# Optimization experiments

Hardware: AMD Instinct MI355X
Metric: run time of the kernel (lower is better)

## Reference

```python
import jax, jax.numpy as jnp
import numpy as np

EMBED_DIM = 512
KDIM = 64
VDIM = 64


def setup_inputs() -> dict:
    key = jax.random.key(0)
    kx, kq, kk, kv = jax.random.split(key, 4)
    B, S = 4, 4096
    x = jax.random.normal(kx, (B, S, EMBED_DIM), dtype=jnp.float32)
    # nn.Linear(embed_dim, out) weight has shape [out, embed_dim]
    WQ = jax.random.normal(kq, (KDIM, EMBED_DIM), dtype=jnp.float32) * (EMBED_DIM ** -0.5)
    WK = jax.random.normal(kk, (KDIM, EMBED_DIM), dtype=jnp.float32) * (EMBED_DIM ** -0.5)
    WV = jax.random.normal(kv, (VDIM, EMBED_DIM), dtype=jnp.float32) * (EMBED_DIM ** -0.5)
    return {"x": x, "WQ": WQ, "WK": WK, "WV": WV}


def reference(x, WQ, WK, WV):
    # q,k: [B,S,kdim]; v: [B,S,vdim] (self-attention: x[0] is x[-1])
    q = jnp.einsum('bse,ke->bsk', x, WQ)
    k = jnp.einsum('bse,ke->bsk', x, WK)
    v = jnp.einsum('bse,ve->bsv', x, WV)
    scale = k.shape[-1] ** -0.5
    scores = jnp.einsum('bqk,bsk->bqs', q, k) * scale  # [B,S,S]
    # dropout p=0.0 -> identity; masked branch in source is a no-op (non-in-place masked_fill discarded)
    attn = jax.nn.softmax(scores, axis=-1)
    out = jnp.einsum('bqs,bsv->bqv', attn, v)  # [B,S,vdim]
    return out
```

## Files before the change

### kernel.cpp

```cpp
#include <hip/hip_runtime.h>

#define BATCH 4
#define SEQ   4096
#define EMB   512
#define HD    64

typedef __attribute__((ext_vector_type(8))) short short8;
typedef __attribute__((ext_vector_type(4))) float floatx4;

static __device__ __forceinline__ unsigned short f2bf(float f) {
  unsigned u = __builtin_bit_cast(unsigned, f);
  u += 0x7fffu + ((u >> 16) & 1u);
  return (unsigned short)(u >> 16);
}
static __device__ __forceinline__ float bf2f(unsigned short h) {
  unsigned u = ((unsigned)h) << 16;
  return __builtin_bit_cast(float, u);
}
static __device__ __forceinline__ unsigned pack_hi16(float lo, float hi) {
#if __has_builtin(__builtin_amdgcn_perm)
  return __builtin_amdgcn_perm(__builtin_bit_cast(unsigned, hi),
                               __builtin_bit_cast(unsigned, lo), 0x07060302u);
#else
  return (__builtin_bit_cast(unsigned, lo) >> 16) |
         (__builtin_bit_cast(unsigned, hi) & 0xffff0000u);
#endif
}
static __device__ __forceinline__ unsigned pack_f16(float a, float b) {
#if __has_builtin(__builtin_amdgcn_cvt_pkrtz)
  typedef __fp16 fp16v2 __attribute__((ext_vector_type(2)));
  fp16v2 h = __builtin_amdgcn_cvt_pkrtz(a, b);
  return __builtin_bit_cast(unsigned, h);
#else
  _Float16 ha = (_Float16)a, hb = (_Float16)b;
  return (unsigned)__builtin_bit_cast(unsigned short, ha) |
         ((unsigned)__builtin_bit_cast(unsigned short, hb) << 16);
#endif
}
static __device__ __forceinline__ float f16_to_f32(unsigned short bits) {
  _Float16 h = __builtin_bit_cast(_Float16, bits);
  return (float)h;
}

__global__ __launch_bounds__(256) void convw_kernel(
    const float* __restrict__ WQ, const float* __restrict__ WK,
    const float* __restrict__ WV, unsigned short* __restrict__ Wpk)
{
  int t = blockIdx.x * 256 + threadIdx.x;
  int p    = t >> 12;
  int w    = (t >> 10) & 3;
  int kc   = (t >> 6) & 15;
  int lane = t & 63;
  int lr = lane & 15, g = lane >> 4;
  const float* src = (p == 0) ? WQ : ((p == 1) ? WK : WV);
  const float4* s4 = (const float4*)(src + (16 * w + lr) * EMB + kc * 32 + 8 * g);
  float4 a = s4[0], b = s4[1];
  float vv[8] = {a.x, a.y, a.z, a.w, b.x, b.y, b.z, b.w};
  short8 o;
#pragma unroll
  for (int j = 0; j < 8; ++j) {
    unsigned short h = f2bf(vv[j]);
    o[j] = (p == 3) ? (short)f2bf(vv[j] - bf2f(h)) : (short)h;
  }
  *(short8*)(Wpk + (size_t)t * 8) = o;
}

#define XST 40

__global__ __launch_bounds__(256) void proj_kernel(
    const float* __restrict__ x,
    const unsigned short* __restrict__ Wpk,
    unsigned short* __restrict__ Qb,
    unsigned short* __restrict__ Kb,
    unsigned short* __restrict__ VTb)
{
  __shared__ __align__(16) unsigned short Xh[2][32 * XST];
  __shared__ __align__(16) unsigned short Xl[2][32 * XST];

  const int tid  = threadIdx.x;
  const int lane = tid & 63;
  const int w    = tid >> 6;
  const int lr   = lane & 15, g = lane >> 4;
  const long rowBase = (long)blockIdx.x * 32;

  floatx4 accQ[2], accK[2], accV[2];
#pragma unroll
  for (int rt = 0; rt < 2; ++rt) {
    floatx4 z = {0.f, 0.f, 0.f, 0.f};
    accQ[rt] = z; accK[rt] = z; accV[rt] = z;
  }

  const int srow = tid >> 3;
  const int sc   = 4 * (tid & 7);
  const float* xbase = x + (rowBase + srow) * EMB + sc;

  auto stage_write = [&](float4 v, int buf) {
    float vv[4] = {v.x, v.y, v.z, v.w};
    ushort4 hi, lo;
#pragma unroll
    for (int i = 0; i < 4; ++i) {
      unsigned short h = f2bf(vv[i]);
      ((unsigned short*)&hi)[i] = h;
      ((unsigned short*)&lo)[i] = f2bf(vv[i] - bf2f(h));
    }
    *(ushort4*)&Xh[buf][srow * XST + sc] = hi;
    *(ushort4*)&Xl[buf][srow * XST + sc] = lo;
  };

  short8 Wb[2][4];
  {
    const unsigned short* wb_ = Wpk + (size_t)(w * 16) * 512 + lane * 8;
    Wb[0][0] = *(const short8*)(wb_);
    Wb[0][1] = *(const short8*)(wb_ + 32768);
    Wb[0][2] = *(const short8*)(wb_ + 2 * 32768);
    Wb[0][3] = *(const short8*)(wb_ + 3 * 32768);
  }

  float4 xv = *(const float4*)(xbase);
  stage_write(xv, 0);
  float4 xn1 = *(const float4*)(xbase + 32);
  float4 xn2 = *(const float4*)(xbase + 64);
  float4 xn3 = *(const float4*)(xbase + 96);

#pragma unroll 2
  for (int kc = 0; kc < 16; ++kc) {
    if (kc + 1 < 16) {
      const unsigned short* wb_ = Wpk + (size_t)(w * 16 + kc + 1) * 512 + lane * 8;
      Wb[(kc + 1) & 1][0] = *(const short8*)(wb_);
      Wb[(kc + 1) & 1][1] = *(const short8*)(wb_ + 32768);
      Wb[(kc + 1) & 1][2] = *(const short8*)(wb_ + 2 * 32768);
      Wb[(kc + 1) & 1][3] = *(const short8*)(wb_ + 3 * 32768);
    }
    float4 xfut;
    if (kc + 4 < 16) xfut = *(const float4*)(xbase + (kc + 4) * 32);
    __syncthreads();
    const int buf = kc & 1;
#pragma unroll
    for (int rt = 0; rt < 2; ++rt) {
      short8 xh = *(const short8*)&Xh[buf][(16 * rt + lr) * XST + 8 * g];
      short8 xl = *(const short8*)&Xl[buf][(16 * rt + lr) * XST + 8 * g];
      accQ[rt] = __builtin_amdgcn_mfma_f32_16x16x32_bf16(Wb[buf][0], xh, accQ[rt], 0, 0, 0);
      accK[rt] = __builtin_amdgcn_mfma_f32_16x16x32_bf16(Wb[buf][1], xh, accK[rt], 0, 0, 0);
      accV[rt] = __builtin_amdgcn_mfma_f32_16x16x32_bf16(xh, Wb[buf][2], accV[rt], 0, 0, 0);
      accV[rt] = __builtin_amdgcn_mfma_f32_16x16x32_bf16(xl, Wb[buf][2], accV[rt], 0, 0, 0);
      accV[rt] = __builtin_amdgcn_mfma_f32_16x16x32_bf16(xh, Wb[buf][3], accV[rt], 0, 0, 0);
    }
    if (kc + 1 < 16) { stage_write(xn1, (kc + 1) & 1); xn1 = xn2; xn2 = xn3; xn3 = xfut; }
  }

  const int bb  = (int)(rowBase >> 12);
  const int sIn = (int)(rowBase & 4095);
#pragma unroll
  for (int rt = 0; rt < 2; ++rt) {
    {
      long row = rowBase + 16 * rt + lr;
      int  col = 16 * w + 4 * g;
      ushort4 u; u.x = f2bf(accQ[rt][0]); u.y = f2bf(accQ[rt][1]);
      u.z = f2bf(accQ[rt][2]); u.w = f2bf(accQ[rt][3]);
      *(ushort4*)(Qb + row * HD + col) = u;
      ushort4 v; v.x = f2bf(accK[rt][0]); v.y = f2bf(accK[rt][1]);
      v.z = f2bf(accK[rt][2]); v.w = f2bf(accK[rt][3]);
      *(ushort4*)(Kb + row * HD + col) = v;
    }
    {
      long addr = ((long)(bb * 64 + 16 * w + lr)) * SEQ + sIn + 16 * rt + 4 * g;
      ushort4 u; u.x = f2bf(accV[rt][0]); u.y = f2bf(accV[rt][1]);
      u.z = f2bf(accV[rt][2]); u.w = f2bf(accV[rt][3]);
      *(ushort4*)(VTb + addr) = u;
    }
  }
}

#define PST 72

__global__ __launch_bounds__(256, 3) void flash_kernel(
    const unsigned short* __restrict__ Qb,
    const unsigned short* __restrict__ Kb,
    const unsigned short* __restrict__ VTb,
    unsigned short* __restrict__ Opart,
    float* __restrict__ Lpart)
{
  __shared__ __align__(16) unsigned short K0lds[64 * 64];
  __shared__ __align__(16) unsigned short V0lds[64 * 64];
  __shared__ __align__(16) unsigned short K1lds[64 * 64];
  __shared__ __align__(16) unsigned short V1lds[64 * 64];
  __shared__ __align__(16) unsigned short Plds[4][32 * PST];

  const int tid  = threadIdx.x;
  const int lane = tid & 63;
  const int w    = tid >> 6;
  const int lr   = lane & 15, g = lane >> 4;
  const int qb2  = blockIdx.x >> 3;
  const int ks   = blockIdx.x & 7;
  const int bb   = qb2 >> 5;
  const long qrow0 = (long)qb2 * 128 + 32 * w;
  const int  kbase = ks * 512;

  short8 qf[2][2];
#pragma unroll
  for (int qh = 0; qh < 2; ++qh)
#pragma unroll
    for (int ec = 0; ec < 2; ++ec)
      qf[qh][ec] = *(const short8*)(Qb + (qrow0 + 16 * qh + lr) * HD + ec * 32 + 8 * g);

  floatx4 accO[2][4];
  floatx4 accL[2];
#pragma unroll
  for (int qh = 0; qh < 2; ++qh) {
    floatx4 z = {0.f, 0.f, 0.f, 0.f};
#pragma unroll
    for (int t = 0; t < 4; ++t) accO[qh][t] = z;
    accL[qh] = z;
  }
  short8 onesf;
#pragma unroll
  for (int j = 0; j < 8; ++j) onesf[j] = (short)0x3F80;

  const float cp = 0.18033688011112042f;
  const float SH = 2.0f;

#define STAGE(kt_, KL, VL) do {                                               \
    const int k0_ = kbase + (kt_) * 64;                                       \
    _Pragma("unroll")                                                         \
    for (int h_ = 0; h_ < 2; ++h_) {                                          \
      int ci_  = h_ * 256 + tid;                                              \
      int row_ = ci_ >> 3;                                                    \
      int cc_  = (ci_ & 7) ^ (row_ & 7);                                      \
      const unsigned short* gK_ = Kb + ((long)bb * SEQ + k0_ + row_) * HD + cc_ * 8; \
      __builtin_amdgcn_global_load_lds(                                       \
          (const __attribute__((address_space(1))) void*)gK_,                 \
          (__attribute__((address_space(3))) void*)((KL) + ci_ * 8), 16, 0, 0); \
      const unsigned short* gV_ = VTb + ((long)bb * HD + row_) * SEQ + k0_ + cc_ * 8; \
      __builtin_amdgcn_global_load_lds(                                       \
          (const __attribute__((address_space(1))) void*)gV_,                 \
          (__attribute__((address_space(3))) void*)((VL) + ci_ * 8), 16, 0, 0); \
    }                                                                         \
  } while (0)

#define COMPUTE(KL, VL) do {                                                  \
    short8 kf[2][4];                                                          \
    _Pragma("unroll")                                                         \
    for (int ec = 0; ec < 2; ++ec)                                            \
      _Pragma("unroll")                                                       \
      for (int t = 0; t < 4; ++t) {                                           \
        int key  = 16 * t + lr;                                               \
        int slot = key * 8 + ((4 * ec + g) ^ (key & 7));                      \
        kf[ec][t] = *(const short8*)((KL) + slot * 8);                        \
      }                                                                       \
    _Pragma("unroll")                                                         \
    for (int qh = 0; qh < 2; ++qh) {                                          \
      floatx4 s_[4];                                                          \
      _Pragma("unroll")                                                       \
      for (int t = 0; t < 4; ++t) { floatx4 z = {0.f,0.f,0.f,0.f}; s_[t] = z; } \
      _Pragma("unroll")                                                       \
      for (int ec = 0; ec < 2; ++ec)                                          \
        _Pragma("unroll")                                                     \
        for (int t = 0; t < 4; ++t)                                           \
          s_[t] = __builtin_amdgcn_mfma_f32_16x16x32_bf16(kf[ec][t], qf[qh][ec], s_[t], 0, 0, 0); \
      unsigned short* prow = &Plds[w][(16 * qh + lr) * PST];                  \
      _Pragma("unroll")                                                       \
      for (int t = 0; t < 4; ++t) {                                           \
        float p0 = __builtin_amdgcn_exp2f(__builtin_fmaf(s_[t][0], cp, -SH)); \
        float p1 = __builtin_amdgcn_exp2f(__builtin_fmaf(s_[t][1], cp, -SH)); \
        float p2 = __builtin_amdgcn_exp2f(__builtin_fmaf(s_[t][2], cp, -SH)); \
        float p3 = __builtin_amdgcn_exp2f(__builtin_fmaf(s_[t][3], cp, -SH)); \
        uint2 u;                                                              \
        u.x = pack_hi16(p0, p1);                                              \
        u.y = pack_hi16(p2, p3);                                              \
        *(uint2*)(prow + 16 * t + 4 * g) = u;                                 \
      }                                                                       \
    }                                                                         \
    short8 vf[2][4];                                                          \
    _Pragma("unroll")                                                         \
    for (int c = 0; c < 2; ++c)                                               \
      _Pragma("unroll")                                                       \
      for (int t = 0; t < 4; ++t) {                                           \
        int d    = 16 * t + lr;                                               \
        int slot = d * 8 + ((4 * c + g) ^ (d & 7));                           \
        vf[c][t] = *(const short8*)((VL) + slot * 8);                         \
      }                                                                       \
    _Pragma("unroll")                                                         \
    for (int qh = 0; qh < 2; ++qh)                                            \
      _Pragma("unroll")                                                       \
      for (int c = 0; c < 2; ++c) {                                           \
        short8 pf = *(const short8*)(&Plds[w][(16 * qh + lr) * PST + 32 * c + 8 * g]); \
        _Pragma("unroll")                                                     \
        for (int t = 0; t < 4; ++t)                                           \
          accO[qh][t] = __builtin_amdgcn_mfma_f32_16x16x32_bf16(vf[c][t], pf, accO[qh][t], 0, 0, 0); \
        accL[qh] = __builtin_amdgcn_mfma_f32_16x16x32_bf16(onesf, pf, accL[qh], 0, 0, 0); \
      }                                                                       \
  } while (0)

  STAGE(0, K0lds, V0lds);
  for (int kt = 0; kt < 8; kt += 2) {
    __syncthreads();
    STAGE(kt + 1, K1lds, V1lds);
    COMPUTE(K0lds, V0lds);
    __syncthreads();
    if (kt + 2 < 8) STAGE(kt + 2, K0lds, V0lds);
    COMPUTE(K1lds, V1lds);
  }
#undef STAGE
#undef COMPUTE

  const int qbOld = qb2 >> 1;
  unsigned short* obase = Opart + (size_t)(qbOld * 8 + ks) * 256 * HD;
#pragma unroll
  for (int qh = 0; qh < 2; ++qh) {
    int qlocal = (qb2 & 1) * 128 + 32 * w + 16 * qh + lr;
#pragma unroll
    for (int t = 0; t < 4; ++t) {
      uint2 u;
      u.x = pack_f16(accO[qh][t][0], accO[qh][t][1]);
      u.y = pack_f16(accO[qh][t][2], accO[qh][t][3]);
      *(uint2*)(obase + qlocal * HD + 16 * t + 4 * g) = u;
    }
    if (g == 0) Lpart[(qbOld * 8 + ks) * 256 + qlocal] = accL[qh][0];
  }
}

__global__ __launch_bounds__(256) void combine_kernel(
    const unsigned short* __restrict__ Opart, const float* __restrict__ Lpart,
    float* __restrict__ out)
{
  int t   = blockIdx.x * 256 + threadIdx.x;
  int row = t >> 4;
  int d0  = (t & 15) * 4;
  int qb = row >> 8, qi = row & 255;
  float4 acc = {0.f, 0.f, 0.f, 0.f};
  float lt = 0.0f;
#pragma unroll
  for (int ks = 0; ks < 8; ++ks) {
    const unsigned short* p = Opart + ((size_t)(qb * 8 + ks) * 256 + qi) * HD + d0;
    ushort4 v = *(const ushort4*)p;
    acc.x += f16_to_f32(v.x);
    acc.y += f16_to_f32(v.y);
    acc.z += f16_to_f32(v.z);
    acc.w += f16_to_f32(v.w);
    lt += Lpart[(qb * 8 + ks) * 256 + qi];
  }
  float inv = 1.0f / lt;
  float4 o = {acc.x * inv, acc.y * inv, acc.z * inv, acc.w * inv};
  *(float4*)(out + (size_t)row * HD + d0) = o;
}

extern "C" void kernel_launch(void* const* d_in, const int* in_sizes, int n_in,
                              void* d_out, int out_size, void* d_ws, size_t ws_size,
                              hipStream_t stream) {
  const float* x  = (const float*)d_in[0];
  const float* WQ = (const float*)d_in[1];
  const float* WK = (const float*)d_in[2];
  const float* WV = (const float*)d_in[3];

  unsigned short* Qb  = (unsigned short*)d_ws;
  unsigned short* Kb  = Qb  + (size_t)BATCH * SEQ * HD;
  unsigned short* VTb = Kb  + (size_t)BATCH * SEQ * HD;
  unsigned short* Wpk = VTb + (size_t)BATCH * SEQ * HD;
  unsigned short* Opart = Wpk + 262144;
  float* Lpart = (float*)(Opart + (size_t)512 * 256 * HD);

  convw_kernel<<<64, 256, 0, stream>>>(WQ, WK, WV, Wpk);
  proj_kernel<<<(BATCH * SEQ) / 32, 256, 0, stream>>>(x, Wpk, Qb, Kb, VTb);
  flash_kernel<<<1024, 256, 0, stream>>>(Qb, Kb, VTb, Opart, Lpart);
  combine_kernel<<<1024, 256, 0, stream>>>(Opart, Lpart, (float*)d_out);
}
```

Measured before the change: 118.2 us.

## Quad-buffer X staging in projection and raise wave priority around attention MFMAs

The projection kernel switches from double-buffered X tiles with register-prefetched weights to four LDS buffers. Two k-chunks are processed per barrier, which halves the number of __syncthreads, and weights are now loaded directly inside the loop instead of being double-buffered in registers. The attention compute macro wraps its MFMA bursts in s_setprio(1)/s_setprio(0) so waves issuing matrix ops get scheduling priority over waves doing exp/LDS work. The changes trade more LDS usage and less explicit weight prefetching for fewer barriers and better MFMA issue interleaving.

```diff
diff --git a/kernel.cpp b/kernel.cpp
--- a/kernel.cpp
+++ b/kernel.cpp
@@ -74,8 +74,8 @@
     unsigned short* __restrict__ Kb,
     unsigned short* __restrict__ VTb)
 {
-  __shared__ __align__(16) unsigned short Xh[2][32 * XST];
-  __shared__ __align__(16) unsigned short Xl[2][32 * XST];
+  __shared__ __align__(16) unsigned short Xh[4][32 * XST];
+  __shared__ __align__(16) unsigned short Xl[4][32 * XST];
 
   const int tid  = threadIdx.x;
   const int lane = tid & 63;
@@ -107,45 +107,43 @@
     *(ushort4*)&Xl[buf][srow * XST + sc] = lo;
   };
 
-  short8 Wb[2][4];
-  {
-    const unsigned short* wb_ = Wpk + (size_t)(w * 16) * 512 + lane * 8;
-    Wb[0][0] = *(const short8*)(wb_);
-    Wb[0][1] = *(const short8*)(wb_ + 32768);
-    Wb[0][2] = *(const short8*)(wb_ + 2 * 32768);
-    Wb[0][3] = *(const short8*)(wb_ + 3 * 32768);
-  }
-
-  float4 xv = *(const float4*)(xbase);
-  stage_write(xv, 0);
-  float4 xn1 = *(const float4*)(xbase + 32);
-  float4 xn2 = *(const float4*)(xbase + 64);
-  float4 xn3 = *(const float4*)(xbase + 96);
-
-#pragma unroll 2
-  for (int kc = 0; kc < 16; ++kc) {
-    if (kc + 1 < 16) {
-      const unsigned short* wb_ = Wpk + (size_t)(w * 16 + kc + 1) * 512 + lane * 8;
-      Wb[(kc + 1) & 1][0] = *(const short8*)(wb_);
-      Wb[(kc + 1) & 1][1] = *(const short8*)(wb_ + 32768);
-      Wb[(kc + 1) & 1][2] = *(const short8*)(wb_ + 2 * 32768);
-      Wb[(kc + 1) & 1][3] = *(const short8*)(wb_ + 3 * 32768);
-    }
-    float4 xfut;
-    if (kc + 4 < 16) xfut = *(const float4*)(xbase + (kc + 4) * 32);
+  float4 x0 = *(const float4*)(xbase);
+  float4 x1 = *(const float4*)(xbase + 32);
+  stage_write(x0, 0);
+  stage_write(x1, 1);
+  float4 xA = *(const float4*)(xbase + 2 * 32);
+  float4 xB = *(const float4*)(xbase + 3 * 32);
+  float4 xC = *(const float4*)(xbase + 4 * 32);
+  float4 xD = *(const float4*)(xbase + 5 * 32);
+
+  for (int kc = 0; kc < 16; kc += 2) {
     __syncthreads();
-    const int buf = kc & 1;
-#pragma unroll
-    for (int rt = 0; rt < 2; ++rt) {
-      short8 xh = *(const short8*)&Xh[buf][(16 * rt + lr) * XST + 8 * g];
-      short8 xl = *(const short8*)&Xl[buf][(16 * rt + lr) * XST + 8 * g];
-      accQ[rt] = __builtin_amdgcn_mfma_f32_16x16x32_bf16(Wb[buf][0], xh, accQ[rt], 0, 0, 0);
-      accK[rt] = __builtin_amdgcn_mfma_f32_16x16x32_bf16(Wb[buf][1], xh, accK[rt], 0, 0, 0);
-      accV[rt] = __builtin_amdgcn_mfma_f32_16x16x32_bf16(xh, Wb[buf][2], accV[rt], 0, 0, 0);
-      accV[rt] = __builtin_amdgcn_mfma_f32_16x16x32_bf16(xl, Wb[buf][2], accV[rt], 0, 0, 0);
-      accV[rt] = __builtin_amdgcn_mfma_f32_16x16x32_bf16(xh, Wb[buf][3], accV[rt], 0, 0, 0);
-    }
-    if (kc + 1 < 16) { stage_write(xn1, (kc + 1) & 1); xn1 = xn2; xn2 = xn3; xn3 = xfut; }
+    if (kc + 2 < 16) { stage_write(xA, (kc + 2) & 3); stage_write(xB, (kc + 3) & 3); }
+    xA = xC; xB = xD;
+    if (kc + 6 < 16) {
+      xC = *(const float4*)(xbase + (kc + 6) * 32);
+      xD = *(const float4*)(xbase + (kc + 7) * 32);
+    }
+#pragma unroll
+    for (int k2 = 0; k2 < 2; ++k2) {
+      const int kcc = kc + k2;
+      const unsigned short* wb_ = Wpk + (size_t)(w * 16 + kcc) * 512 + lane * 8;
+      short8 wq  = *(const short8*)(wb_);
+      short8 wk  = *(const short8*)(wb_ + 32768);
+      short8 wvh = *(const short8*)(wb_ + 2 * 32768);
+      short8 wvl = *(const short8*)(wb_ + 3 * 32768);
+      const int buf = kcc & 3;
+#pragma unroll
+      for (int rt = 0; rt < 2; ++rt) {
+        short8 xh = *(const short8*)&Xh[buf][(16 * rt + lr) * XST + 8 * g];
+        short8 xl = *(const short8*)&Xl[buf][(16 * rt + lr) * XST + 8 * g];
+        accQ[rt] = __builtin_amdgcn_mfma_f32_16x16x32_bf16(wq,  xh, accQ[rt], 0, 0, 0);
+        accK[rt] = __builtin_amdgcn_mfma_f32_16x16x32_bf16(wk,  xh, accK[rt], 0, 0, 0);
+        accV[rt] = __builtin_amdgcn_mfma_f32_16x16x32_bf16(xh, wvh, accV[rt], 0, 0, 0);
+        accV[rt] = __builtin_amdgcn_mfma_f32_16x16x32_bf16(xl, wvh, accV[rt], 0, 0, 0);
+        accV[rt] = __builtin_amdgcn_mfma_f32_16x16x32_bf16(xh, wvl, accV[rt], 0, 0, 0);
+      }
+    }
   }
 
   const int bb  = (int)(rowBase >> 12);
@@ -252,11 +250,13 @@
       floatx4 s_[4];                                                          \
       _Pragma("unroll")                                                       \
       for (int t = 0; t < 4; ++t) { floatx4 z = {0.f,0.f,0.f,0.f}; s_[t] = z; } \
+      __builtin_amdgcn_s_setprio(1);                                          \
       _Pragma("unroll")                                                       \
       for (int ec = 0; ec < 2; ++ec)                                          \
         _Pragma("unroll")                                                     \
         for (int t = 0; t < 4; ++t)                                           \
           s_[t] = __builtin_amdgcn_mfma_f32_16x16x32_bf16(kf[ec][t], qf[qh][ec], s_[t], 0, 0, 0); \
+      __builtin_amdgcn_s_setprio(0);                                          \
       unsigned short* prow = &Plds[w][(16 * qh + lr) * PST];                  \
       _Pragma("unroll")                                                       \
       for (int t = 0; t < 4; ++t) {                                           \
@@ -284,10 +284,12 @@
       _Pragma("unroll")                                                       \
       for (int c = 0; c < 2; ++c) {                                           \
         short8 pf = *(const short8*)(&Plds[w][(16 * qh + lr) * PST + 32 * c + 8 * g]); \
+        __builtin_amdgcn_s_setprio(1);                                        \
         _Pragma("unroll")                                                     \
         for (int t = 0; t < 4; ++t)                                           \
           accO[qh][t] = __builtin_amdgcn_mfma_f32_16x16x32_bf16(vf[c][t], pf, accO[qh][t], 0, 0, 0); \
         accL[qh] = __builtin_amdgcn_mfma_f32_16x16x32_bf16(onesf, pf, accL[qh], 0, 0, 0); \
+        __builtin_amdgcn_s_setprio(0);                                        \
       }                                                                       \
   } while (0)
 
```

Result: no change. 118.7 us (+0.4%).
